# Kernel optimization log

Hardware: AMD Instinct MI355X
Metric: run time of the kernel (lower is better)

Reference implementation:

```python
import jax, jax.numpy as jnp
import numpy as np

NUM_CAPSULE = 16
DIM_CAPSULE = 64
ROUTINGS = 3
T_EPS = 1e-07


def squash(v, axis=-1):
    # NOTE: this repo's 'squash' is v / sqrt(||v||^2 + eps) (norm-only scaling)
    s = jnp.sum(v * v, axis=axis, keepdims=True)
    return v / jnp.sqrt(s + T_EPS)


def setup_inputs() -> dict:
    key = jax.random.key(0)
    k1, k2 = jax.random.split(key)
    B, N_in, D_in = 64, 512, 1024
    x = jax.random.normal(k1, (B, N_in, D_in), dtype=jnp.float32)
    # xavier-normal-ish init for W [1, D_in, num_capsule*dim_capsule]
    fan_in, fan_out = D_in, NUM_CAPSULE * DIM_CAPSULE
    std = float(np.sqrt(2.0 / (fan_in + fan_out)))
    W = jax.random.normal(k2, (1, D_in, NUM_CAPSULE * DIM_CAPSULE), dtype=jnp.float32) * std
    return {"x": x, "W": W}


def reference(x, W):
    B, N_in, D_in = x.shape
    # u_hat: [B, N_in, num_cap*dim_cap] -> [B, num_cap, N_in, dim_cap]
    u_hat = jnp.matmul(x, W[0])
    u_hat = u_hat.reshape(B, N_in, NUM_CAPSULE, DIM_CAPSULE).transpose(0, 2, 1, 3)
    b = jnp.zeros((B, NUM_CAPSULE, N_in), dtype=u_hat.dtype)
    outputs = None
    for i in range(ROUTINGS):
        # torch code permutes to [B, N_in, num_cap], softmaxes dim=2, permutes back:
        # equivalent to softmax over the num_capsule axis (axis=1)
        c = jax.nn.softmax(b, axis=1)  # [B, num_cap, N_in]
        outputs = squash(jnp.einsum('bij,bijk->bik', c, u_hat))  # [B, num_cap, dim_cap]
        if i < ROUTINGS - 1:
            b = jnp.einsum('bik,bijk->bij', outputs, u_hat)  # [B, num_cap, N_in]
    return outputs
```

## Files before the change

kernel.cpp:

```cpp
#include <hip/hip_runtime.h>
#include <stdint.h>

#define NUM_CAP 16
#define DIM_CAP 64
#define BATCH   64
#define N_IN    512
#define D_IN    1024
#define N_COL   1024
#define M_ROWS  (BATCH*N_IN)

typedef __attribute__((ext_vector_type(8))) short short8;
typedef __attribute__((ext_vector_type(4))) float f32x4;

__device__ __forceinline__ float bf2f(unsigned int u) {
  return __uint_as_float(u << 16);
}
__device__ __forceinline__ unsigned short f2bf_rne(float f) {
  unsigned int x = __float_as_uint(f);
  x += 0x7fffu + ((x >> 16) & 1u);
  return (unsigned short)(x >> 16);
}
__device__ __forceinline__ unsigned int pack_trunc(unsigned int lo, unsigned int hi) {
  return (lo >> 16) | (hi & 0xffff0000u);
}

__global__ void transpose_w(const float* __restrict__ W,
                            unsigned short* __restrict__ Wt) {
  __shared__ float tile[32][33];
  const int tx = threadIdx.x, ty = threadIdx.y;
  const int bx = blockIdx.x, by = blockIdx.y;
  tile[ty][tx] = W[(by * 32 + ty) * N_COL + bx * 32 + tx];
  __syncthreads();
  Wt[(bx * 32 + ty) * D_IN + by * 32 + tx] = f2bf_rne(tile[tx][ty]);
}

__global__ __launch_bounds__(256) void gemm_uhat(
    const float* __restrict__ A,
    const unsigned short* __restrict__ Bt,
    unsigned short* __restrict__ C) {
  __shared__ __align__(16) unsigned short lA[128 * 32];
  __shared__ __align__(16) unsigned short lB[128 * 32];

  const int t = threadIdx.x;
  const int wave = t >> 6, lane = t & 63;
  const int xcd = blockIdx.x & 7, local = blockIdx.x >> 3;
  const int mt = xcd * 32 + (local >> 3), nt = local & 7;
  const int m0 = mt * 128, n0 = nt * 128;
  const int wm = wave & 1, wn = wave >> 1;

  f32x4 acc[4][4] = {};

  const int ar = t >> 1, ah = t & 1;
  const float* agp = A + (size_t)(m0 + ar) * D_IN + ah * 16;
  const int xrA = (ar >> 1) & 3;
  unsigned short* lap0 = lA + ar * 32 + ((2 * ah + 0) ^ xrA) * 8;
  unsigned short* lap1 = lA + ar * 32 + ((2 * ah + 1) ^ xrA) * 8;

  const int srow = lane >> 2;
  const int schunk = ((lane & 3) ^ ((srow >> 1) & 3)) * 8;

  uint4 a0 = *(const uint4*)(agp);
  uint4 a1 = *(const uint4*)(agp + 4);
  uint4 a2 = *(const uint4*)(agp + 8);
  uint4 a3 = *(const uint4*)(agp + 12);

  for (int kt = 0; kt < D_IN / 32; ++kt) {
    const int k0 = kt * 32;
    __syncthreads();
    uint4 p0, p1;
    p0.x = pack_trunc(a0.x, a0.y); p0.y = pack_trunc(a0.z, a0.w);
    p0.z = pack_trunc(a1.x, a1.y); p0.w = pack_trunc(a1.z, a1.w);
    p1.x = pack_trunc(a2.x, a2.y); p1.y = pack_trunc(a2.z, a2.w);
    p1.z = pack_trunc(a3.x, a3.y); p1.w = pack_trunc(a3.z, a3.w);
    *(uint4*)lap0 = p0;
    *(uint4*)lap1 = p1;
    #pragma unroll
    for (int s0 = 0; s0 < 2; ++s0) {
      const int s = wave + s0 * 4;
      const unsigned short* gb = Bt + (size_t)(n0 + s * 16 + srow) * D_IN + k0 + schunk;
      __builtin_amdgcn_global_load_lds(
          (const __attribute__((address_space(1))) void*)gb,
          (__attribute__((address_space(3))) void*)(lB + s * 512), 16, 0, 0);
    }
    __syncthreads();

    const int kn = ((kt + 1) & 31) * 32;
    a0 = *(const uint4*)(agp + kn);
    a1 = *(const uint4*)(agp + kn + 4);
    a2 = *(const uint4*)(agp + kn + 8);
    a3 = *(const uint4*)(agp + kn + 12);

    short8 af[4], bfr[4];
    const int rsel = lane & 15;
    const int q = lane >> 4;
    const int koff = (q ^ ((rsel >> 1) & 3)) * 8;
    #pragma unroll
    for (int tm = 0; tm < 4; tm++)
      af[tm] = *(const short8*)&lA[(wm * 64 + tm * 16 + rsel) * 32 + koff];
    #pragma unroll
    for (int tn = 0; tn < 4; tn++)
      bfr[tn] = *(const short8*)&lB[(wn * 64 + tn * 16 + rsel) * 32 + koff];
    #pragma unroll
    for (int tm = 0; tm < 4; tm++)
      #pragma unroll
      for (int tn = 0; tn < 4; tn++)
        acc[tm][tn] = __builtin_amdgcn_mfma_f32_16x16x32_bf16(
            af[tm], bfr[tn], acc[tm][tn], 0, 0, 0);
  }

  const int lrow = (lane >> 4) * 4, lcol = lane & 15;
  #pragma unroll
  for (int tm = 0; tm < 4; tm++)
    #pragma unroll
    for (int tn = 0; tn < 4; tn++)
      #pragma unroll
      for (int r = 0; r < 4; r++) {
        const int row = m0 + wm * 64 + tm * 16 + lrow + r;
        const int col = n0 + wn * 64 + tn * 16 + lcol;
        C[(size_t)row * N_COL + col] = f2bf_rne(acc[tm][tn][r]);
      }
}

__global__ __launch_bounds__(1024) void route_all(
    const unsigned short* __restrict__ uhat,
    float* __restrict__ out) {
  __shared__ float red[16][1028];
  __shared__ float sq[16][68];
  const int t = threadIdx.x;
  const int w = t >> 6, lane = t & 63;
  const int b = blockIdx.x;
  const int i_l = lane >> 2, c4 = lane & 3;
  const int oi = t >> 6, ok = t & 63;

  const unsigned short* ub0 =
      uhat + (size_t)(b * N_IN + w * 32) * N_COL + lane * 16;

  for (int it = 0; it < 3; ++it) {
    float pv[16];
    if (it) {
      #pragma unroll
      for (int q = 0; q < 4; q++)
        *(float4*)&pv[q * 4] = *(const float4*)&sq[i_l][c4 * 16 + q * 4];
    }
    float acc[16];
    #pragma unroll
    for (int q = 0; q < 16; q++) acc[q] = 0.f;

    const unsigned short* ub = ub0;
    for (int jj = 0; jj < 32; ++jj, ub += N_COL) {
      const uint4 d0 = *(const uint4*)ub;
      const uint4 d1 = *(const uint4*)(ub + 8);
      float u[16];
      #define UNP(wd, o) { u[(o)] = bf2f((wd) & 0xffffu); u[(o)+1] = __uint_as_float((wd) & 0xffff0000u); }
      UNP(d0.x, 0) UNP(d0.y, 2) UNP(d0.z, 4) UNP(d0.w, 6)
      UNP(d1.x, 8) UNP(d1.y, 10) UNP(d1.z, 12) UNP(d1.w, 14)
      #undef UNP

      float c;
      if (it == 0) {
        c = 0.0625f;
      } else {
        float dot = 0.f;
        #pragma unroll
        for (int q = 0; q < 16; q++) dot = fmaf(pv[q], u[q], dot);
        dot += __shfl_xor(dot, 1);
        dot += __shfl_xor(dot, 2);
        float m = dot;
        #pragma unroll
        for (int d = 4; d < 64; d <<= 1) m = fmaxf(m, __shfl_xor(m, d));
        const float e = __expf(dot - m);
        float s = e;
        #pragma unroll
        for (int d = 4; d < 64; d <<= 1) s += __shfl_xor(s, d);
        c = e / s;
      }
      #pragma unroll
      for (int q = 0; q < 16; q++) acc[q] = fmaf(c, u[q], acc[q]);
    }

    #pragma unroll
    for (int q = 0; q < 4; q++)
      *(float4*)&red[w][i_l * 64 + c4 * 16 + q * 4] = make_float4(
          acc[q * 4 + 0], acc[q * 4 + 1], acc[q * 4 + 2], acc[q * 4 + 3]);
    __syncthreads();

    float s = 0.f;
    #pragma unroll
    for (int ww = 0; ww < 16; ++ww) s += red[ww][t];

    float ss = s * s;
    #pragma unroll
    for (int d = 1; d < 64; d <<= 1) ss += __shfl_xor(ss, d);
    const float v = s / sqrtf(ss + 1e-7f);

    __syncthreads();
    if (it < 2) {
      sq[oi][ok] = v;
      __syncthreads();
    } else {
      out[b * 1024 + t] = v;
    }
  }
}

extern "C" void kernel_launch(void* const* d_in, const int* in_sizes, int n_in,
                              void* d_out, int out_size, void* d_ws, size_t ws_size,
                              hipStream_t stream) {
  const float* x = (const float*)d_in[0];
  const float* W = (const float*)d_in[1];
  float* out = (float*)d_out;

  char* ws = (char*)d_ws;
  unsigned short* Wt   = (unsigned short*)ws;
  unsigned short* uhat = (unsigned short*)(ws + (size_t)(2 << 20));

  transpose_w<<<dim3(32, 32), dim3(32, 32), 0, stream>>>(W, Wt);
  gemm_uhat<<<2048, 256, 0, stream>>>(x, Wt, uhat);
  route_all<<<BATCH, 1024, 0, stream>>>(uhat, out);
}
```

Measured before the change: 371.9 us.

## Factor routing through W to avoid materializing u_hat

Drops the full u_hat GEMM and its bf16 intermediate. Routing is re-expressed algebraically: the iteration-0 sum uses the row-sum of x times W, the agreement logits use x·(W·v), and the weighted sums use (c^T x)·W, all in fp32 with CUDA-core FMAs. This removes the large u_hat write and reads and the bf16 precision loss, but it re-reads x (128MB) about five times across eight launches and gives up the MFMA path.

```diff
diff --git a/kernel.cpp b/kernel.cpp
--- a/kernel.cpp
+++ b/kernel.cpp
@@ -7,200 +7,158 @@
 #define N_IN    512
 #define D_IN    1024
 #define N_COL   1024
-#define M_ROWS  (BATCH*N_IN)
 
-typedef __attribute__((ext_vector_type(8))) short short8;
-typedef __attribute__((ext_vector_type(4))) float f32x4;
 
-__device__ __forceinline__ float bf2f(unsigned int u) {
-  return __uint_as_float(u << 16);
-}
-__device__ __forceinline__ unsigned short f2bf_rne(float f) {
-  unsigned int x = __float_as_uint(f);
-  x += 0x7fffu + ((x >> 16) & 1u);
-  return (unsigned short)(x >> 16);
-}
-__device__ __forceinline__ unsigned int pack_trunc(unsigned int lo, unsigned int hi) {
-  return (lo >> 16) | (hi & 0xffff0000u);
+__global__ __launch_bounds__(256) void k_xsum(const float* __restrict__ x,
+                                              float* __restrict__ xsum4) {
+  const int b = blockIdx.x >> 2, jc = blockIdx.x & 3;
+  const int t = threadIdx.x;
+  const float* xp = x + ((size_t)(b * 512 + jc * 128)) * 1024 + t * 4;
+  float4 a = make_float4(0.f, 0.f, 0.f, 0.f);
+  #pragma unroll 4
+  for (int j = 0; j < 128; ++j, xp += 1024) {
+    const float4 v = *(const float4*)xp;
+    a.x += v.x; a.y += v.y; a.z += v.z; a.w += v.w;
+  }
+  *(float4*)&xsum4[(size_t)blockIdx.x * 1024 + t * 4] = a;
 }
 
-__global__ void transpose_w(const float* __restrict__ W,
-                            unsigned short* __restrict__ Wt) {
-  __shared__ float tile[32][33];
-  const int tx = threadIdx.x, ty = threadIdx.y;
-  const int bx = blockIdx.x, by = blockIdx.y;
-  tile[ty][tx] = W[(by * 32 + ty) * N_COL + bx * 32 + tx];
+__global__ __launch_bounds__(64) void k_vw(
+    const float* __restrict__ W, const float* __restrict__ xsum4,
+    const float* __restrict__ spart, float* __restrict__ wtg,
+    float* __restrict__ out, const int smode, const int wmode) {
+  __shared__ float xsl[1024];
+  __shared__ float vls[64];
+  __shared__ float wbuf[1024];
+  const int bi = blockIdx.x, b = bi >> 4, i = bi & 15;
+  const int lane = threadIdx.x;
+
+  float s;
+  if (smode == 0) {
+    const float* xs = xsum4 + (size_t)b * 4096;
+    #pragma unroll
+    for (int it = 0; it < 16; ++it) {
+      const int d = it * 64 + lane;
+      xsl[d] = xs[d] + xs[1024 + d] + xs[2048 + d] + xs[3072 + d];
+    }
+    __syncthreads();
+    s = 0.f;
+    const float* wp = W + i * 64 + lane;
+    #pragma unroll 8
+    for (int d = 0; d < 1024; ++d)
+      s = fmaf(xsl[d], wp[(size_t)d * 1024], s);
+    s *= 0.0625f;
+  } else {
+    const float* sp = spart + (size_t)b * 4096 + i * 64 + lane;
+    s = sp[0] + sp[1024] + sp[2048] + sp[3072];
+  }
+
+  float ss = s * s;
+  #pragma unroll
+  for (int d = 1; d < 64; d <<= 1) ss += __shfl_xor(ss, d);
+  const float v = s / sqrtf(ss + 1e-7f);
+
+  if (wmode == 0) { out[(size_t)bi * 64 + lane] = v; return; }
+
+  vls[lane] = v;
   __syncthreads();
-  Wt[(bx * 32 + ty) * D_IN + by * 32 + tx] = f2bf_rne(tile[tx][ty]);
+  const int dq = lane >> 4, kq = lane & 15;
+  const float4 vk = *(const float4*)&vls[kq * 4];
+  for (int db = 0; db < 1024; db += 4) {
+    const int d = db + dq;
+    const float4 wr = *(const float4*)&W[(size_t)d * 1024 + i * 64 + kq * 4];
+    float p = wr.x * vk.x + wr.y * vk.y + wr.z * vk.z + wr.w * vk.w;
+    p += __shfl_xor(p, 1); p += __shfl_xor(p, 2);
+    p += __shfl_xor(p, 4); p += __shfl_xor(p, 8);
+    if (kq == 0) wbuf[d] = p;
+  }
+  __syncthreads();
+  float* wo = wtg + (size_t)bi * 1024;
+  #pragma unroll
+  for (int it = 0; it < 16; ++it) wo[it * 64 + lane] = wbuf[it * 64 + lane];
 }
 
-__global__ __launch_bounds__(256) void gemm_uhat(
-    const float* __restrict__ A,
-    const unsigned short* __restrict__ Bt,
-    unsigned short* __restrict__ C) {
-  __shared__ __align__(16) unsigned short lA[128 * 32];
-  __shared__ __align__(16) unsigned short lB[128 * 32];
+__global__ __launch_bounds__(256) void k_B(
+    const float* __restrict__ x, const float* __restrict__ wtg,
+    float* __restrict__ cg) {
+  __shared__ float wl[16 * 1024];
+  const int b = blockIdx.x >> 5, jc = blockIdx.x & 31;
+  const int t = threadIdx.x, jl = t >> 4, i = t & 15;
 
-  const int t = threadIdx.x;
-  const int wave = t >> 6, lane = t & 63;
-  const int xcd = blockIdx.x & 7, local = blockIdx.x >> 3;
-  const int mt = xcd * 32 + (local >> 3), nt = local & 7;
-  const int m0 = mt * 128, n0 = nt * 128;
-  const int wm = wave & 1, wn = wave >> 1;
+  const float4* src = (const float4*)(wtg + (size_t)b * 16384);
+  #pragma unroll
+  for (int it = 0; it < 16; ++it) {
+    const int f4 = it * 256 + t;
+    *(float4*)&wl[it * 1024 + (t ^ it) * 4] = src[f4];
+  }
+  __syncthreads();
 
-  f32x4 acc[4][4] = {};
-
-  const int ar = t >> 1, ah = t & 1;
-  const float* agp = A + (size_t)(m0 + ar) * D_IN + ah * 16;
-  const int xrA = (ar >> 1) & 3;
-  unsigned short* lap0 = lA + ar * 32 + ((2 * ah + 0) ^ xrA) * 8;
-  unsigned short* lap1 = lA + ar * 32 + ((2 * ah + 1) ^ xrA) * 8;
-
-  const int srow = lane >> 2;
-  const int schunk = ((lane & 3) ^ ((srow >> 1) & 3)) * 8;
-
-  uint4 a0 = *(const uint4*)(agp);
-  uint4 a1 = *(const uint4*)(agp + 4);
-  uint4 a2 = *(const uint4*)(agp + 8);
-  uint4 a3 = *(const uint4*)(agp + 12);
-
-  for (int kt = 0; kt < D_IN / 32; ++kt) {
-    const int k0 = kt * 32;
-    __syncthreads();
-    uint4 p0, p1;
-    p0.x = pack_trunc(a0.x, a0.y); p0.y = pack_trunc(a0.z, a0.w);
-    p0.z = pack_trunc(a1.x, a1.y); p0.w = pack_trunc(a1.z, a1.w);
-    p1.x = pack_trunc(a2.x, a2.y); p1.y = pack_trunc(a2.z, a2.w);
-    p1.z = pack_trunc(a3.x, a3.y); p1.w = pack_trunc(a3.z, a3.w);
-    *(uint4*)lap0 = p0;
-    *(uint4*)lap1 = p1;
-    #pragma unroll
-    for (int s0 = 0; s0 < 2; ++s0) {
-      const int s = wave + s0 * 4;
-      const unsigned short* gb = Bt + (size_t)(n0 + s * 16 + srow) * D_IN + k0 + schunk;
-      __builtin_amdgcn_global_load_lds(
-          (const __attribute__((address_space(1))) void*)gb,
-          (__attribute__((address_space(3))) void*)(lB + s * 512), 16, 0, 0);
-    }
-    __syncthreads();
-
-    const int kn = ((kt + 1) & 31) * 32;
-    a0 = *(const uint4*)(agp + kn);
-    a1 = *(const uint4*)(agp + kn + 4);
-    a2 = *(const uint4*)(agp + kn + 8);
-    a3 = *(const uint4*)(agp + kn + 12);
-
-    short8 af[4], bfr[4];
-    const int rsel = lane & 15;
-    const int q = lane >> 4;
-    const int koff = (q ^ ((rsel >> 1) & 3)) * 8;
-    #pragma unroll
-    for (int tm = 0; tm < 4; tm++)
-      af[tm] = *(const short8*)&lA[(wm * 64 + tm * 16 + rsel) * 32 + koff];
-    #pragma unroll
-    for (int tn = 0; tn < 4; tn++)
-      bfr[tn] = *(const short8*)&lB[(wn * 64 + tn * 16 + rsel) * 32 + koff];
-    #pragma unroll
-    for (int tm = 0; tm < 4; tm++)
-      #pragma unroll
-      for (int tn = 0; tn < 4; tn++)
-        acc[tm][tn] = __builtin_amdgcn_mfma_f32_16x16x32_bf16(
-            af[tm], bfr[tn], acc[tm][tn], 0, 0, 0);
+  const int j = jc * 16 + jl;
+  const float* xp = x + ((size_t)(b * 512 + j)) * 1024;
+  float acc = 0.f;
+  #pragma unroll 4
+  for (int d = 0; d < 1024; d += 4) {
+    const float4 xv = *(const float4*)(xp + d);
+    const float4 wv = *(const float4*)&wl[i * 1024 + (((d >> 2)) ^ i) * 4];
+    acc = fmaf(xv.x, wv.x, acc); acc = fmaf(xv.y, wv.y, acc);
+    acc = fmaf(xv.z, wv.z, acc); acc = fmaf(xv.w, wv.w, acc);
   }
-
-  const int lrow = (lane >> 4) * 4, lcol = lane & 15;
-  #pragma unroll
-  for (int tm = 0; tm < 4; tm++)
-    #pragma unroll
-    for (int tn = 0; tn < 4; tn++)
-      #pragma unroll
-      for (int r = 0; r < 4; r++) {
-        const int row = m0 + wm * 64 + tm * 16 + lrow + r;
-        const int col = n0 + wn * 64 + tn * 16 + lcol;
-        C[(size_t)row * N_COL + col] = f2bf_rne(acc[tm][tn][r]);
-      }
+  const float e = __expf(acc);
+  float se = e;
+  se += __shfl_xor(se, 1); se += __shfl_xor(se, 2);
+  se += __shfl_xor(se, 4); se += __shfl_xor(se, 8);
+  cg[(size_t)b * 8192 + jc * 256 + t] = e / se;
 }
 
-__global__ __launch_bounds__(1024) void route_all(
-    const unsigned short* __restrict__ uhat,
-    float* __restrict__ out) {
-  __shared__ float red[16][1028];
-  __shared__ float sq[16][68];
+__global__ __launch_bounds__(256) void k_ys(
+    const float* __restrict__ x, const float* __restrict__ cg,
+    const float* __restrict__ W, float* __restrict__ spart) {
+  __shared__ float cl[512 * 16];
+  __shared__ float yl[16 * 260];
+  const int b = blockIdx.x >> 2, dc = blockIdx.x & 3;
   const int t = threadIdx.x;
-  const int w = t >> 6, lane = t & 63;
-  const int b = blockIdx.x;
-  const int i_l = lane >> 2, c4 = lane & 3;
-  const int oi = t >> 6, ok = t & 63;
 
-  const unsigned short* ub0 =
-      uhat + (size_t)(b * N_IN + w * 32) * N_COL + lane * 16;
+  const float4* csrc = (const float4*)(cg + (size_t)b * 8192);
+  #pragma unroll
+  for (int it = 0; it < 8; ++it)
+    *(float4*)&cl[(it * 256 + t) * 4] = csrc[it * 256 + t];
+  __syncthreads();
 
-  for (int it = 0; it < 3; ++it) {
-    float pv[16];
-    if (it) {
-      #pragma unroll
-      for (int q = 0; q < 4; q++)
-        *(float4*)&pv[q * 4] = *(const float4*)&sq[i_l][c4 * 16 + q * 4];
-    }
-    float acc[16];
-    #pragma unroll
-    for (int q = 0; q < 16; q++) acc[q] = 0.f;
+  float acc[16];
+  #pragma unroll
+  for (int q = 0; q < 16; ++q) acc[q] = 0.f;
+  const float* xp = x + (size_t)b * 512 * 1024 + dc * 256 + t;
+  #pragma unroll 2
+  for (int j = 0; j < 512; ++j) {
+    const float xv = xp[(size_t)j * 1024];
+    const float4 c0 = *(const float4*)&cl[j * 16];
+    const float4 c1 = *(const float4*)&cl[j * 16 + 4];
+    const float4 c2 = *(const float4*)&cl[j * 16 + 8];
+    const float4 c3 = *(const float4*)&cl[j * 16 + 12];
+    acc[0]  = fmaf(c0.x, xv, acc[0]);  acc[1]  = fmaf(c0.y, xv, acc[1]);
+    acc[2]  = fmaf(c0.z, xv, acc[2]);  acc[3]  = fmaf(c0.w, xv, acc[3]);
+    acc[4]  = fmaf(c1.x, xv, acc[4]);  acc[5]  = fmaf(c1.y, xv, acc[5]);
+    acc[6]  = fmaf(c1.z, xv, acc[6]);  acc[7]  = fmaf(c1.w, xv, acc[7]);
+    acc[8]  = fmaf(c2.x, xv, acc[8]);  acc[9]  = fmaf(c2.y, xv, acc[9]);
+    acc[10] = fmaf(c2.z, xv, acc[10]); acc[11] = fmaf(c2.w, xv, acc[11]);
+    acc[12] = fmaf(c3.x, xv, acc[12]); acc[13] = fmaf(c3.y, xv, acc[13]);
+    acc[14] = fmaf(c3.z, xv, acc[14]); acc[15] = fmaf(c3.w, xv, acc[15]);
+  }
+  #pragma unroll
+  for (int q = 0; q < 16; ++q) yl[q * 260 + t] = acc[q];
+  __syncthreads();
 
-    const unsigned short* ub = ub0;
-    for (int jj = 0; jj < 32; ++jj, ub += N_COL) {
-      const uint4 d0 = *(const uint4*)ub;
-      const uint4 d1 = *(const uint4*)(ub + 8);
-      float u[16];
-      #define UNP(wd, o) { u[(o)] = bf2f((wd) & 0xffffu); u[(o)+1] = __uint_as_float((wd) & 0xffff0000u); }
-      UNP(d0.x, 0) UNP(d0.y, 2) UNP(d0.z, 4) UNP(d0.w, 6)
-      UNP(d1.x, 8) UNP(d1.y, 10) UNP(d1.z, 12) UNP(d1.w, 14)
-      #undef UNP
-
-      float c;
-      if (it == 0) {
-        c = 0.0625f;
-      } else {
-        float dot = 0.f;
-        #pragma unroll
-        for (int q = 0; q < 16; q++) dot = fmaf(pv[q], u[q], dot);
-        dot += __shfl_xor(dot, 1);
-        dot += __shfl_xor(dot, 2);
-        float m = dot;
-        #pragma unroll
-        for (int d = 4; d < 64; d <<= 1) m = fmaxf(m, __shfl_xor(m, d));
-        const float e = __expf(dot - m);
-        float s = e;
-        #pragma unroll
-        for (int d = 4; d < 64; d <<= 1) s += __shfl_xor(s, d);
-        c = e / s;
-      }
-      #pragma unroll
-      for (int q = 0; q < 16; q++) acc[q] = fmaf(c, u[q], acc[q]);
-    }
-
-    #pragma unroll
-    for (int q = 0; q < 4; q++)
-      *(float4*)&red[w][i_l * 64 + c4 * 16 + q * 4] = make_float4(
-          acc[q * 4 + 0], acc[q * 4 + 1], acc[q * 4 + 2], acc[q * 4 + 3]);
-    __syncthreads();
-
-    float s = 0.f;
-    #pragma unroll
-    for (int ww = 0; ww < 16; ++ww) s += red[ww][t];
-
-    float ss = s * s;
-    #pragma unroll
-    for (int d = 1; d < 64; d <<= 1) ss += __shfl_xor(ss, d);
-    const float v = s / sqrtf(ss + 1e-7f);
-
-    __syncthreads();
-    if (it < 2) {
-      sq[oi][ok] = v;
-      __syncthreads();
-    } else {
-      out[b * 1024 + t] = v;
-    }
+  const int i = t >> 4, kq = t & 15;
+  float4 sa = make_float4(0.f, 0.f, 0.f, 0.f);
+  const float* wp = W + (size_t)(dc * 256) * 1024 + i * 64 + kq * 4;
+  #pragma unroll 4
+  for (int dl = 0; dl < 256; ++dl) {
+    const float yv = yl[i * 260 + dl];
+    const float4 wv = *(const float4*)(wp + (size_t)dl * 1024);
+    sa.x = fmaf(yv, wv.x, sa.x); sa.y = fmaf(yv, wv.y, sa.y);
+    sa.z = fmaf(yv, wv.z, sa.z); sa.w = fmaf(yv, wv.w, sa.w);
   }
+  *(float4*)&spart[((size_t)b * 4 + dc) * 1024 + i * 64 + kq * 4] = sa;
 }
 
 extern "C" void kernel_launch(void* const* d_in, const int* in_sizes, int n_in,
@@ -211,10 +169,17 @@
   float* out = (float*)d_out;
 
   char* ws = (char*)d_ws;
-  unsigned short* Wt   = (unsigned short*)ws;
-  unsigned short* uhat = (unsigned short*)(ws + (size_t)(2 << 20));
+  float* xsum4 = (float*)ws;
+  float* wtg   = (float*)(ws + (size_t)2  * (1 << 20));
+  float* cg    = (float*)(ws + (size_t)8  * (1 << 20));
+  float* spart = (float*)(ws + (size_t)12 * (1 << 20));
 
-  transpose_w<<<dim3(32, 32), dim3(32, 32), 0, stream>>>(W, Wt);
-  gemm_uhat<<<2048, 256, 0, stream>>>(x, Wt, uhat);
-  route_all<<<BATCH, 1024, 0, stream>>>(uhat, out);
+  k_xsum<<<256, 256, 0, stream>>>(x, xsum4);
+  k_vw<<<1024, 64, 0, stream>>>(W, xsum4, spart, wtg, out, 0, 1);
+  k_B <<<2048, 256, 0, stream>>>(x, wtg, cg);
+  k_ys<<<256, 256, 0, stream>>>(x, cg, W, spart);
+  k_vw<<<1024, 64, 0, stream>>>(W, xsum4, spart, wtg, out, 1, 1);
+  k_B <<<2048, 256, 0, stream>>>(x, wtg, cg);
+  k_ys<<<256, 256, 0, stream>>>(x, cg, W, spart);
+  k_vw<<<1024, 64, 0, stream>>>(W, xsum4, spart, wtg, out, 1, 0);
 }
```

Result: slower. 791.3 us (+112.8%).
